# Kernel tuning notes

Measured on AMD Instinct MI355X. Metric: run time of the kernel, lower is better.

The kernel has to match this reference:

```python
import jax, jax.numpy as jnp
import numpy as np

C = 64  # in_dim

def _dwpw(x, w_dw, w_pw):
    # depthwise 1x1x1 conv (groups=C, no bias) == per-channel scale
    x = x * w_dw[None, :, None, None, None]
    # pointwise 1x1x1 conv (no bias) == channel mixing matmul
    return jnp.einsum('bcdhw,oc->bodhw', x, w_pw)

def setup_inputs() -> dict:
    key = jax.random.key(0)
    ks = jax.random.split(key, 8)
    B, D, H, W = 2, 16, 16, 16
    x = jax.random.normal(ks[0], (B, C, D, H, W), dtype=jnp.float32)
    s = 1.0 / np.sqrt(C)
    q_dw = jax.random.normal(ks[1], (C,), dtype=jnp.float32) * s
    q_pw = jax.random.normal(ks[2], (C, C), dtype=jnp.float32) * s
    k_dw = jax.random.normal(ks[3], (C,), dtype=jnp.float32) * s
    k_pw = jax.random.normal(ks[4], (C, C), dtype=jnp.float32) * s
    v_dw = jax.random.normal(ks[5], (C,), dtype=jnp.float32) * s
    v_pw = jax.random.normal(ks[6], (C, C), dtype=jnp.float32) * s
    gamma = jnp.zeros((1,), dtype=jnp.float32) + 0.1  # nonzero so output depends on attention
    return {"x": x, "q_dw": q_dw, "q_pw": q_pw, "k_dw": k_dw, "k_pw": k_pw,
            "v_dw": v_dw, "v_pw": v_pw, "gamma": gamma}

def reference(x, q_dw, q_pw, k_dw, k_pw, v_dw, v_pw, gamma):
    B, Cc, D, H, W = x.shape
    N = D * H * W
    q = _dwpw(x, q_dw, q_pw).reshape(B, Cc, N)  # [B,C,N]
    k = _dwpw(x, k_dw, k_pw).reshape(B, Cc, N)
    v = _dwpw(x, v_dw, v_pw).reshape(B, Cc, N)
    # energy[b,i,j] = sum_c q[b,c,i] * k[b,c,j]
    energy = jnp.einsum('bci,bcj->bij', q, k)
    attn = jax.nn.softmax(energy, axis=-1)  # softmax over j
    # out[b,c,i] = sum_j v[b,c,j] * attn[b,i,j]
    out = jnp.einsum('bcj,bij->bci', v, attn).reshape(B, Cc, D, H, W)
    return gamma * out + x
```

## Files before the change

kernel.cpp:

```cpp
#include <hip/hip_runtime.h>
#include <hip/hip_bf16.h>

#define NPOS 4096
#define CDIM 64
#define BATCH 2
#define JSPLIT 8
#define JSHIFT 3
#define JCHUNK (NPOS / JSPLIT)
#define NTILE (JCHUNK / 64)
#define RPB 64

typedef __attribute__((ext_vector_type(8))) short bf16x8;
typedef __attribute__((ext_vector_type(4))) short short4b;
typedef __attribute__((ext_vector_type(4))) float f32x4;
typedef __attribute__((ext_vector_type(4))) unsigned int u32x4;
typedef __attribute__((ext_vector_type(2))) unsigned int u32x2;

static __device__ __forceinline__ unsigned int fbits(float f) {
    union { float f; unsigned int u; } v; v.f = f; return v.u;
}
static __device__ __forceinline__ float bffloat(unsigned int hi16) {
    union { unsigned int u; float f; } v; v.u = hi16; return v.f;
}
static __device__ __forceinline__ unsigned int pk2bf(float a, float b) {
    return ((fbits(a) + 0x8000u) >> 16) | ((fbits(b) + 0x8000u) & 0xffff0000u);
}
static __device__ __forceinline__ short f2bs(float f) {
    return (short)(unsigned short)((fbits(f) + 0x8000u) >> 16);
}

static __device__ __forceinline__ void gload16(const void* g, void* l) {
    __builtin_amdgcn_global_load_lds(
        (const __attribute__((address_space(1))) unsigned int*)g,
        (__attribute__((address_space(3))) unsigned int*)l, 16, 0, 0);
}

__global__ __launch_bounds__(64) void qkv_kernel(
    const float* __restrict__ x,
    const float* __restrict__ q_dw, const float* __restrict__ q_pw,
    const float* __restrict__ k_dw, const float* __restrict__ k_pw,
    const float* __restrict__ v_dw, const float* __restrict__ v_pw,
    short* __restrict__ qT, short* __restrict__ kT, short* __restrict__ vM)
{
    const int bid  = blockIdx.x;
    const int p    = bid >> 9;
    const int np   = bid & 511;
    const int b    = np >> 8;
    const int n0   = (np & 255) << 4;
    const int lane = threadIdx.x;
    const int col  = lane & 15;
    const int quad = lane >> 4;
    const int n    = n0 + col;

    const float* pw = (p == 0) ? q_pw : (p == 1) ? k_pw : v_pw;
    const float* dw = (p == 0) ? q_dw : (p == 1) ? k_dw : v_dw;

    bf16x8 xf0, xf1;
    float dv0[8], dv1[8];
    #pragma unroll
    for (int j = 0; j < 8; ++j) {
        xf0[j] = f2bs(x[(size_t)(b * CDIM + quad * 8 + j) * NPOS + n]);
        xf1[j] = f2bs(x[(size_t)(b * CDIM + 32 + quad * 8 + j) * NPOS + n]);
        dv0[j] = dw[quad * 8 + j];
        dv1[j] = dw[32 + quad * 8 + j];
    }

    #pragma unroll
    for (int os = 0; os < 4; ++os) {
        const float* pr = pw + (os * 16 + col) * 64 + quad * 8;
        bf16x8 wf0, wf1;
        #pragma unroll
        for (int j = 0; j < 8; ++j) {
            wf0[j] = f2bs(pr[j] * dv0[j]);
            wf1[j] = f2bs(pr[32 + j] * dv1[j]);
        }
        f32x4 d = (f32x4){0.f, 0.f, 0.f, 0.f};
        if (p < 2) {
            d = __builtin_amdgcn_mfma_f32_16x16x32_bf16(wf0, xf0, d, 0, 0, 0);
            d = __builtin_amdgcn_mfma_f32_16x16x32_bf16(wf1, xf1, d, 0, 0, 0);
            short* dst = p ? kT : qT;
            *(u32x2*)(dst + (size_t)(b * NPOS + n) * CDIM + os * 16 + quad * 4) =
                (u32x2){pk2bf(d[0], d[1]), pk2bf(d[2], d[3])};
        } else {
            d = __builtin_amdgcn_mfma_f32_16x16x32_bf16(xf0, wf0, d, 0, 0, 0);
            d = __builtin_amdgcn_mfma_f32_16x16x32_bf16(xf1, wf1, d, 0, 0, 0);
            *(u32x2*)(vM + (size_t)(b * CDIM + os * 16 + col) * NPOS + n0 + quad * 4) =
                (u32x2){pk2bf(d[0], d[1]), pk2bf(d[2], d[3])};
        }
    }
}

__global__ __launch_bounds__(256, 4) void attn_kernel(
    const short* __restrict__ qT, const short* __restrict__ kT,
    const short* __restrict__ vM,
    unsigned short* __restrict__ Opart, float* __restrict__ lacc)
{
    const int gid  = blockIdx.x;
    const int jc   = gid & (JSPLIT - 1);
    const int rb   = (gid >> JSHIFT) & 63;
    const int b    = gid >> (JSHIFT + 6);
    const int t    = threadIdx.x;
    const int wave = t >> 6;
    const int lane = t & 63;
    const int col  = lane & 15;
    const int quad = lane >> 4;

    __shared__ __align__(16) short Kbuf[2][64 * 64];
    __shared__ __align__(16) short Vbuf[2][64 * 64];
    __shared__ __align__(16) short Pw[4][16 * 64];

    const short* qTb = qT + (size_t)b * NPOS * CDIM;
    const char*  kTB = (const char*)(kT + (size_t)b * NPOS * CDIM);
    const char*  vB  = (const char*)(vM + (size_t)b * CDIM * NPOS);

    const int i0 = rb * RPB + wave * 16;

    auto stage = [&](int tt) {
        const int j0 = jc * JCHUNK + tt * 64;
        const char* kS = kTB + (size_t)j0 * (CDIM * 2);
        const char* vS = vB  + (size_t)j0 * 2;
        char* kD = (char*)&Kbuf[tt & 1][0];
        char* vD = (char*)&Vbuf[tt & 1][0];
        #pragma unroll
        for (int i = 0; i < 2; ++i) {
            const int base = wave * 2048 + i * 1024;
            const int L    = base + lane * 16;
            const int r    = L >> 7;
            const int o    = (L & 127) ^ ((r & 7) << 4);
            gload16(kS + (size_t)((L & ~127) + o), kD + base);
            gload16(vS + (size_t)r * (NPOS * 2) + o, vD + base);
        }
    };

    bf16x8 qf[2];
    {
        const short* qp = qTb + (size_t)(i0 + col) * CDIM + quad * 8;
        qf[0] = *(const bf16x8*)qp;
        qf[1] = *(const bf16x8*)(qp + 32);
    }

    f32x4 oacc[4];
    #pragma unroll
    for (int cb = 0; cb < 4; ++cb) oacc[cb] = (f32x4){0.f, 0.f, 0.f, 0.f};
    float lp = 0.f;

    char* Pc = (char*)&Pw[wave][0];
    const int pswz = (col & 7) << 4;
    const int slot = (quad * 16) ^ pswz;

    stage(0);
    __syncthreads();

    for (int tt = 0; tt < NTILE; ++tt) {
        if (tt + 1 < NTILE) stage(tt + 1);

        const char* Kc = (const char*)&Kbuf[tt & 1][0];
        const char* Vc = (const char*)&Vbuf[tt & 1][0];

        #pragma unroll
        for (int ct = 0; ct < 4; ++ct) {
            const char* kr = Kc + (ct * 16 + col) * 128;
            bf16x8 k0 = *(const bf16x8*)(kr + slot);
            bf16x8 k1 = *(const bf16x8*)(kr + (slot ^ 64));
            f32x4 a = (f32x4){0.f, 0.f, 0.f, 0.f};
            __builtin_amdgcn_s_setprio(1);
            a = __builtin_amdgcn_mfma_f32_16x16x32_bf16(k0, qf[0], a, 0, 0, 0);
            a = __builtin_amdgcn_mfma_f32_16x16x32_bf16(k1, qf[1], a, 0, 0, 0);
            __builtin_amdgcn_s_setprio(0);
            float p0 = __expf(a[0]), p1 = __expf(a[1]);
            float p2 = __expf(a[2]), p3 = __expf(a[3]);
            lp += (p0 + p1) + (p2 + p3);
            *(short4b*)(Pc + col * 128 + ((ct * 32 + quad * 8) ^ pswz)) =
                (short4b){f2bs(p0), f2bs(p1), f2bs(p2), f2bs(p3)};
        }

        bf16x8 pf0 = *(const bf16x8*)(Pc + col * 128 + slot);
        bf16x8 pf1 = *(const bf16x8*)(Pc + col * 128 + (slot ^ 64));

        #pragma unroll
        for (int cb = 0; cb < 4; ++cb) {
            const char* vr = Vc + (cb * 16 + col) * 128;
            bf16x8 v0 = *(const bf16x8*)(vr + slot);
            bf16x8 v1 = *(const bf16x8*)(vr + (slot ^ 64));
            __builtin_amdgcn_s_setprio(1);
            oacc[cb] = __builtin_amdgcn_mfma_f32_16x16x32_bf16(v0, pf0, oacc[cb], 0, 0, 0);
            oacc[cb] = __builtin_amdgcn_mfma_f32_16x16x32_bf16(v1, pf1, oacc[cb], 0, 0, 0);
            __builtin_amdgcn_s_setprio(0);
        }
        __syncthreads();
    }

    lp += __shfl_xor(lp, 16, 64);
    lp += __shfl_xor(lp, 32, 64);
    if (quad == 0)
        lacc[(size_t)(jc * BATCH + b) * NPOS + i0 + col] = lp;

    unsigned short* Ob = Opart + (size_t)(jc * BATCH + b) * CDIM * NPOS;
    #pragma unroll
    for (int cb = 0; cb < 4; ++cb)
        #pragma unroll
        for (int r = 0; r < 4; ++r)
            Ob[(size_t)(cb * 16 + quad * 4 + r) * NPOS + i0 + col] =
                (unsigned short)f2bs(oacc[cb][r]);
}

__global__ __launch_bounds__(256) void combine_kernel(
    const unsigned short* __restrict__ Opart, const float* __restrict__ lacc,
    const float* __restrict__ x, const float* __restrict__ gamma,
    float* __restrict__ out)
{
    int b  = blockIdx.x >> 7;
    int n0 = (blockIdx.x & 127) << 5;
    __shared__ float linv[32];
    int t = threadIdx.x;
    if (t < 32) {
        float s = 0.f;
        #pragma unroll
        for (int jc = 0; jc < JSPLIT; ++jc)
            s += lacc[(size_t)(jc * BATCH + b) * NPOS + n0 + t];
        linv[t] = gamma[0] / s;
    }
    __syncthreads();

    int c = t >> 2, ns = (t & 3) * 8;
    float acc[8];
    #pragma unroll
    for (int k = 0; k < 8; ++k) acc[k] = 0.f;
    #pragma unroll
    for (int jc = 0; jc < JSPLIT; ++jc) {
        const unsigned short* Ob = Opart + ((size_t)(jc * BATCH + b) * CDIM + c) * NPOS + n0 + ns;
        u32x4 w = *(const u32x4*)Ob;
        #pragma unroll
        for (int j = 0; j < 4; ++j) {
            acc[2 * j]     += bffloat(w[j] << 16);
            acc[2 * j + 1] += bffloat(w[j] & 0xffff0000u);
        }
    }
    const float* xb = x + ((size_t)b * CDIM + c) * NPOS + n0 + ns;
    float* ob = out + ((size_t)b * CDIM + c) * NPOS + n0 + ns;
    #pragma unroll
    for (int k = 0; k < 2; ++k) {
        f32x4 x4 = *(const f32x4*)(xb + k * 4);
        f32x4 r;
        #pragma unroll
        for (int j = 0; j < 4; ++j)
            r[j] = fmaf(acc[k * 4 + j], linv[ns + k * 4 + j], x4[j]);
        *(f32x4*)(ob + k * 4) = r;
    }
}

extern "C" void kernel_launch(void* const* d_in, const int* in_sizes, int n_in,
                              void* d_out, int out_size, void* d_ws, size_t ws_size,
                              hipStream_t stream) {
    const float* x     = (const float*)d_in[0];
    const float* q_dw  = (const float*)d_in[1];
    const float* q_pw  = (const float*)d_in[2];
    const float* k_dw  = (const float*)d_in[3];
    const float* k_pw  = (const float*)d_in[4];
    const float* v_dw  = (const float*)d_in[5];
    const float* v_pw  = (const float*)d_in[6];
    const float* gamma = (const float*)d_in[7];
    float* out = (float*)d_out;

    char* ws = (char*)d_ws;
    short* qT             = (short*)(ws);
    short* kT             = (short*)(ws + (1u << 20));
    short* vM             = (short*)(ws + (2u << 20));
    unsigned short* Opart = (unsigned short*)(ws + (3u << 20));
    float* lacc           = (float*)(ws + (3u << 20) +
                                     (size_t)JSPLIT * BATCH * CDIM * NPOS * 2);

    qkv_kernel<<<3 * BATCH * 256, 64, 0, stream>>>(
        x, q_dw, q_pw, k_dw, k_pw, v_dw, v_pw, qT, kT, vM);
    attn_kernel<<<BATCH * (NPOS / RPB) * JSPLIT, 256, 0, stream>>>(qT, kT, vM, Opart, lacc);
    combine_kernel<<<BATCH * 128, 256, 0, stream>>>(Opart, lacc, x, gamma, out);
}
```

Baseline: 97.47 us.

## Fuse QKV projection and attention into one cooperative kernel with grid sync

```diff
diff --git a/kernel.cpp b/kernel.cpp
--- a/kernel.cpp
+++ b/kernel.cpp
@@ -1,5 +1,8 @@
 #include <hip/hip_runtime.h>
 #include <hip/hip_bf16.h>
+#include <hip/hip_cooperative_groups.h>
+
+namespace cg = cooperative_groups;
 
 #define NPOS 4096
 #define CDIM 64
@@ -9,6 +12,7 @@
 #define JCHUNK (NPOS / JSPLIT)
 #define NTILE (JCHUNK / 64)
 #define RPB 64
+#define COOP_GRID (BATCH * (NPOS / RPB) * JSPLIT)
 
 typedef __attribute__((ext_vector_type(8))) short bf16x8;
 typedef __attribute__((ext_vector_type(4))) short short4b;
@@ -35,19 +39,18 @@
         (__attribute__((address_space(3))) unsigned int*)l, 16, 0, 0);
 }
 
-__global__ __launch_bounds__(64) void qkv_kernel(
+static __device__ __forceinline__ void qkv_body(
+    int u, int lane,
     const float* __restrict__ x,
     const float* __restrict__ q_dw, const float* __restrict__ q_pw,
     const float* __restrict__ k_dw, const float* __restrict__ k_pw,
     const float* __restrict__ v_dw, const float* __restrict__ v_pw,
     short* __restrict__ qT, short* __restrict__ kT, short* __restrict__ vM)
 {
-    const int bid  = blockIdx.x;
-    const int p    = bid >> 9;
-    const int np   = bid & 511;
+    const int p    = u >> 9;
+    const int np   = u & 511;
     const int b    = np >> 8;
     const int n0   = (np & 255) << 4;
-    const int lane = threadIdx.x;
     const int col  = lane & 15;
     const int quad = lane >> 4;
     const int n    = n0 + col;
@@ -88,6 +91,143 @@
                 (u32x2){pk2bf(d[0], d[1]), pk2bf(d[2], d[3])};
         }
     }
+}
+
+__global__ __launch_bounds__(256, 4) void pam_fused(
+    const float* __restrict__ x,
+    const float* __restrict__ q_dw, const float* __restrict__ q_pw,
+    const float* __restrict__ k_dw, const float* __restrict__ k_pw,
+    const float* __restrict__ v_dw, const float* __restrict__ v_pw,
+    short* __restrict__ qT, short* __restrict__ kT, short* __restrict__ vM,
+    unsigned short* __restrict__ Opart, float* __restrict__ lacc)
+{
+    const int bid  = blockIdx.x;
+    const int t    = threadIdx.x;
+    const int wave = t >> 6;
+    const int lane = t & 63;
+    const int col  = lane & 15;
+    const int quad = lane >> 4;
+
+    __shared__ __align__(16) short Kbuf[2][64 * 64];
+    __shared__ __align__(16) short Vbuf[2][64 * 64];
+    __shared__ __align__(16) short Pw[4][16 * 64];
+
+    {
+        const int u = wave * 1024 + bid;
+        if (u < 1536)
+            qkv_body(u, lane, x, q_dw, q_pw, k_dw, k_pw, v_dw, v_pw, qT, kT, vM);
+    }
+    __threadfence();
+    cg::this_grid().sync();
+
+    const int jc   = bid & (JSPLIT - 1);
+    const int rb   = (bid >> JSHIFT) & 63;
+    const int b    = bid >> (JSHIFT + 6);
+
+    const short* qTb = qT + (size_t)b * NPOS * CDIM;
+    const char*  kTB = (const char*)(kT + (size_t)b * NPOS * CDIM);
+    const char*  vB  = (const char*)(vM + (size_t)b * CDIM * NPOS);
+
+    const int i0 = rb * RPB + wave * 16;
+
+    auto stage = [&](int tt) {
+        const int j0 = jc * JCHUNK + tt * 64;
+        const char* kS = kTB + (size_t)j0 * (CDIM * 2);
+        const char* vS = vB  + (size_t)j0 * 2;
+        char* kD = (char*)&Kbuf[tt & 1][0];
+        char* vD = (char*)&Vbuf[tt & 1][0];
+        #pragma unroll
+        for (int i = 0; i < 2; ++i) {
+            const int base = wave * 2048 + i * 1024;
+            const int L    = base + lane * 16;
+            const int r    = L >> 7;
+            const int o    = (L & 127) ^ ((r & 7) << 4);
+            gload16(kS + (size_t)((L & ~127) + o), kD + base);
+            gload16(vS + (size_t)r * (NPOS * 2) + o, vD + base);
+        }
+    };
+
+    bf16x8 qf[2];
+    {
+        const short* qp = qTb + (size_t)(i0 + col) * CDIM + quad * 8;
+        qf[0] = *(const bf16x8*)qp;
+        qf[1] = *(const bf16x8*)(qp + 32);
+    }
+
+    f32x4 oacc[4];
+    #pragma unroll
+    for (int cb = 0; cb < 4; ++cb) oacc[cb] = (f32x4){0.f, 0.f, 0.f, 0.f};
+    float lp = 0.f;
+
+    char* Pc = (char*)&Pw[wave][0];
+    const int pswz = (col & 7) << 4;
+    const int slot = (quad * 16) ^ pswz;
+
+    stage(0);
+    __syncthreads();
+
+    for (int tt = 0; tt < NTILE; ++tt) {
+        if (tt + 1 < NTILE) stage(tt + 1);
+
+        const char* Kc = (const char*)&Kbuf[tt & 1][0];
+        const char* Vc = (const char*)&Vbuf[tt & 1][0];
+
+        #pragma unroll
+        for (int ct = 0; ct < 4; ++ct) {
+            const char* kr = Kc + (ct * 16 + col) * 128;
+            bf16x8 k0 = *(const bf16x8*)(kr + slot);
+            bf16x8 k1 = *(const bf16x8*)(kr + (slot ^ 64));
+            f32x4 a = (f32x4){0.f, 0.f, 0.f, 0.f};
+            __builtin_amdgcn_s_setprio(1);
+            a = __builtin_amdgcn_mfma_f32_16x16x32_bf16(k0, qf[0], a, 0, 0, 0);
+            a = __builtin_amdgcn_mfma_f32_16x16x32_bf16(k1, qf[1], a, 0, 0, 0);
+            __builtin_amdgcn_s_setprio(0);
+            float p0 = __expf(a[0]), p1 = __expf(a[1]);
+            float p2 = __expf(a[2]), p3 = __expf(a[3]);
+            lp += (p0 + p1) + (p2 + p3);
+            *(short4b*)(Pc + col * 128 + ((ct * 32 + quad * 8) ^ pswz)) =
+                (short4b){f2bs(p0), f2bs(p1), f2bs(p2), f2bs(p3)};
+        }
+
+        bf16x8 pf0 = *(const bf16x8*)(Pc + col * 128 + slot);
+        bf16x8 pf1 = *(const bf16x8*)(Pc + col * 128 + (slot ^ 64));
+
+        #pragma unroll
+        for (int cb = 0; cb < 4; ++cb) {
+            const char* vr = Vc + (cb * 16 + col) * 128;
+            bf16x8 v0 = *(const bf16x8*)(vr + slot);
+            bf16x8 v1 = *(const bf16x8*)(vr + (slot ^ 64));
+            __builtin_amdgcn_s_setprio(1);
+            oacc[cb] = __builtin_amdgcn_mfma_f32_16x16x32_bf16(v0, pf0, oacc[cb], 0, 0, 0);
+            oacc[cb] = __builtin_amdgcn_mfma_f32_16x16x32_bf16(v1, pf1, oacc[cb], 0, 0, 0);
+            __builtin_amdgcn_s_setprio(0);
+        }
+        __syncthreads();
+    }
+
+    lp += __shfl_xor(lp, 16, 64);
+    lp += __shfl_xor(lp, 32, 64);
+    if (quad == 0)
+        lacc[(size_t)(jc * BATCH + b) * NPOS + i0 + col] = lp;
+
+    unsigned short* Ob = Opart + (size_t)(jc * BATCH + b) * CDIM * NPOS;
+    #pragma unroll
+    for (int cb = 0; cb < 4; ++cb)
+        #pragma unroll
+        for (int r = 0; r < 4; ++r)
+            Ob[(size_t)(cb * 16 + quad * 4 + r) * NPOS + i0 + col] =
+                (unsigned short)f2bs(oacc[cb][r]);
+}
+
+__global__ __launch_bounds__(64) void qkv_kernel(
+    const float* __restrict__ x,
+    const float* __restrict__ q_dw, const float* __restrict__ q_pw,
+    const float* __restrict__ k_dw, const float* __restrict__ k_pw,
+    const float* __restrict__ v_dw, const float* __restrict__ v_pw,
+    short* __restrict__ qT, short* __restrict__ kT, short* __restrict__ vM)
+{
+    qkv_body(blockIdx.x, threadIdx.x, x, q_dw, q_pw, k_dw, k_pw, v_dw, v_pw,
+             qT, kT, vM);
 }
 
 __global__ __launch_bounds__(256, 4) void attn_kernel(
@@ -270,8 +410,18 @@
     float* lacc           = (float*)(ws + (3u << 20) +
                                      (size_t)JSPLIT * BATCH * CDIM * NPOS * 2);
 
-    qkv_kernel<<<3 * BATCH * 256, 64, 0, stream>>>(
-        x, q_dw, q_pw, k_dw, k_pw, v_dw, v_pw, qT, kT, vM);
-    attn_kernel<<<BATCH * (NPOS / RPB) * JSPLIT, 256, 0, stream>>>(qT, kT, vM, Opart, lacc);
+    void* args[] = {
+        (void*)&x, (void*)&q_dw, (void*)&q_pw, (void*)&k_dw, (void*)&k_pw,
+        (void*)&v_dw, (void*)&v_pw, (void*)&qT, (void*)&kT, (void*)&vM,
+        (void*)&Opart, (void*)&lacc
+    };
+    hipError_t err = hipLaunchCooperativeKernel(
+        (void*)pam_fused, dim3(COOP_GRID), dim3(256), args, 0, stream);
+    if (err != hipSuccess) {
+        (void)hipGetLastError();
+        qkv_kernel<<<3 * BATCH * 256, 64, 0, stream>>>(
+            x, q_dw, q_pw, k_dw, k_pw, v_dw, v_pw, qT, kT, vM);
+        attn_kernel<<<COOP_GRID, 256, 0, stream>>>(qT, kT, vM, Opart, lacc);
+    }
     combine_kernel<<<BATCH * 128, 256, 0, stream>>>(Opart, lacc, x, gamma, out);
 }
```

Result: slower. 238.4 us (+144.6%).

## Fuse split-K combine into attention kernel via last-block atomic counter

Applied to the files above, without the earlier changes.

```diff
diff --git a/kernel.cpp b/kernel.cpp
--- a/kernel.cpp
+++ b/kernel.cpp
@@ -9,6 +9,8 @@
 #define JCHUNK (NPOS / JSPLIT)
 #define NTILE (JCHUNK / 64)
 #define RPB 64
+#define NGROUP (BATCH * (NPOS / RPB))
+#define ATTN_GRID (BATCH * (NPOS / RPB) * JSPLIT)
 
 typedef __attribute__((ext_vector_type(8))) short bf16x8;
 typedef __attribute__((ext_vector_type(4))) short short4b;
@@ -40,14 +42,19 @@
     const float* __restrict__ q_dw, const float* __restrict__ q_pw,
     const float* __restrict__ k_dw, const float* __restrict__ k_pw,
     const float* __restrict__ v_dw, const float* __restrict__ v_pw,
-    short* __restrict__ qT, short* __restrict__ kT, short* __restrict__ vM)
+    short* __restrict__ qT, short* __restrict__ kT, short* __restrict__ vM,
+    int* __restrict__ cnt)
 {
     const int bid  = blockIdx.x;
+    const int lane = threadIdx.x;
+    if (bid == 0) {
+        cnt[lane] = 0;
+        cnt[lane + 64] = 0;
+    }
     const int p    = bid >> 9;
     const int np   = bid & 511;
     const int b    = np >> 8;
     const int n0   = (np & 255) << 4;
-    const int lane = threadIdx.x;
     const int col  = lane & 15;
     const int quad = lane >> 4;
     const int n    = n0 + col;
@@ -93,7 +100,10 @@
 __global__ __launch_bounds__(256, 4) void attn_kernel(
     const short* __restrict__ qT, const short* __restrict__ kT,
     const short* __restrict__ vM,
-    unsigned short* __restrict__ Opart, float* __restrict__ lacc)
+    unsigned short* __restrict__ Opart, float* __restrict__ lacc,
+    int* __restrict__ cnt,
+    const float* __restrict__ x, const float* __restrict__ gamma,
+    float* __restrict__ out)
 {
     const int gid  = blockIdx.x;
     const int jc   = gid & (JSPLIT - 1);
@@ -202,50 +212,55 @@
         for (int r = 0; r < 4; ++r)
             Ob[(size_t)(cb * 16 + quad * 4 + r) * NPOS + i0 + col] =
                 (unsigned short)f2bs(oacc[cb][r]);
-}
-
-__global__ __launch_bounds__(256) void combine_kernel(
-    const unsigned short* __restrict__ Opart, const float* __restrict__ lacc,
-    const float* __restrict__ x, const float* __restrict__ gamma,
-    float* __restrict__ out)
-{
-    int b  = blockIdx.x >> 7;
-    int n0 = (blockIdx.x & 127) << 5;
-    __shared__ float linv[32];
-    int t = threadIdx.x;
-    if (t < 32) {
-        float s = 0.f;
-        #pragma unroll
-        for (int jc = 0; jc < JSPLIT; ++jc)
-            s += lacc[(size_t)(jc * BATCH + b) * NPOS + n0 + t];
-        linv[t] = gamma[0] / s;
-    }
+
     __syncthreads();
-
-    int c = t >> 2, ns = (t & 3) * 8;
-    float acc[8];
-    #pragma unroll
-    for (int k = 0; k < 8; ++k) acc[k] = 0.f;
-    #pragma unroll
-    for (int jc = 0; jc < JSPLIT; ++jc) {
-        const unsigned short* Ob = Opart + ((size_t)(jc * BATCH + b) * CDIM + c) * NPOS + n0 + ns;
-        u32x4 w = *(const u32x4*)Ob;
-        #pragma unroll
-        for (int j = 0; j < 4; ++j) {
-            acc[2 * j]     += bffloat(w[j] << 16);
-            acc[2 * j + 1] += bffloat(w[j] & 0xffff0000u);
-        }
-    }
-    const float* xb = x + ((size_t)b * CDIM + c) * NPOS + n0 + ns;
-    float* ob = out + ((size_t)b * CDIM + c) * NPOS + n0 + ns;
-    #pragma unroll
-    for (int k = 0; k < 2; ++k) {
-        f32x4 x4 = *(const f32x4*)(xb + k * 4);
-        f32x4 r;
-        #pragma unroll
-        for (int j = 0; j < 4; ++j)
-            r[j] = fmaf(acc[k * 4 + j], linv[ns + k * 4 + j], x4[j]);
-        *(f32x4*)(ob + k * 4) = r;
+    int* flag = (int*)&Pw[2][0];
+    if (t == 0) {
+        __threadfence();
+        *flag = atomicAdd(&cnt[b * 64 + rb], 1);
+    }
+    __syncthreads();
+    if (*flag == JSPLIT - 1) {
+        __threadfence();
+        float* linv_s = (float*)&Pw[0][0];
+        const int ib = rb * RPB;
+        if (t < RPB) {
+            float s = 0.f;
+            #pragma unroll
+            for (int j2 = 0; j2 < JSPLIT; ++j2)
+                s += lacc[(size_t)(j2 * BATCH + b) * NPOS + ib + t];
+            linv_s[t] = gamma[0] / s;
+        }
+        __syncthreads();
+        const int c = t >> 2, r0 = (t & 3) * 16;
+        float acc2[16];
+        #pragma unroll
+        for (int k = 0; k < 16; ++k) acc2[k] = 0.f;
+        #pragma unroll
+        for (int j2 = 0; j2 < JSPLIT; ++j2) {
+            const unsigned short* Ob2 = Opart +
+                ((size_t)(j2 * BATCH + b) * CDIM + c) * NPOS + ib + r0;
+            u32x4 w0 = *(const u32x4*)Ob2;
+            u32x4 w1 = *(const u32x4*)(Ob2 + 8);
+            #pragma unroll
+            for (int j = 0; j < 4; ++j) {
+                acc2[2 * j]     += bffloat(w0[j] << 16);
+                acc2[2 * j + 1] += bffloat(w0[j] & 0xffff0000u);
+                acc2[8 + 2 * j] += bffloat(w1[j] << 16);
+                acc2[9 + 2 * j] += bffloat(w1[j] & 0xffff0000u);
+            }
+        }
+        const float* xb = x + ((size_t)b * CDIM + c) * NPOS + ib + r0;
+        float* ob = out + ((size_t)b * CDIM + c) * NPOS + ib + r0;
+        #pragma unroll
+        for (int k = 0; k < 4; ++k) {
+            f32x4 x4 = *(const f32x4*)(xb + k * 4);
+            f32x4 r;
+            #pragma unroll
+            for (int j = 0; j < 4; ++j)
+                r[j] = fmaf(acc2[k * 4 + j], linv_s[r0 + k * 4 + j], x4[j]);
+            *(f32x4*)(ob + k * 4) = r;
+        }
     }
 }
 
@@ -269,9 +284,10 @@
     unsigned short* Opart = (unsigned short*)(ws + (3u << 20));
     float* lacc           = (float*)(ws + (3u << 20) +
                                      (size_t)JSPLIT * BATCH * CDIM * NPOS * 2);
+    int* cnt              = (int*)(ws + (12u << 20));
 
     qkv_kernel<<<3 * BATCH * 256, 64, 0, stream>>>(
-        x, q_dw, q_pw, k_dw, k_pw, v_dw, v_pw, qT, kT, vM);
-    attn_kernel<<<BATCH * (NPOS / RPB) * JSPLIT, 256, 0, stream>>>(qT, kT, vM, Opart, lacc);
-    combine_kernel<<<BATCH * 128, 256, 0, stream>>>(Opart, lacc, x, gamma, out);
-}
+        x, q_dw, q_pw, k_dw, k_pw, v_dw, v_pw, qT, kT, vM, cnt);
+    attn_kernel<<<ATTN_GRID, 256, 0, stream>>>(qT, kT, vM, Opart, lacc,
+                                               cnt, x, gamma, out);
+}
```

Measured after the change: 172.6 us. +77.0%, slower.
